# Kernel tuning notes

Hardware: AMD Instinct MI355X
Metric: run time of the kernel (lower is better)

The kernel has to match this reference:

```python
import jax, jax.numpy as jnp
import numpy as np

N_NODES = 50000
N_EDGES = 800000
D_IN, D_HID, D_OUT = 16, 64, 16
N_BLOCKS = 4


def setup_inputs() -> dict:
    key = jax.random.key(0)
    ks = jax.random.split(key, 12)
    s = 0.05  # small init scale to keep sum-aggregation over 4 blocks stable
    return {
        "x": jax.random.normal(ks[0], (N_NODES, D_IN), jnp.float32),
        "lframes": jax.random.normal(ks[1], (N_NODES, 4, 4), jnp.float32),
        "edge_index": jax.random.randint(ks[2], (2, N_EDGES), 0, N_NODES, jnp.int64),
        "lin_in_w": jax.random.normal(ks[3], (D_IN, D_HID), jnp.float32) * s,
        "lin_in_b": jnp.zeros((D_HID,), jnp.float32),
        # per-block mlp1: Linear(2D->D), ReLU, Linear(D->D), ReLU, Linear(D->D)
        "w0": jax.random.normal(ks[4], (N_BLOCKS, 2 * D_HID, D_HID), jnp.float32) * s,
        "b0": jnp.zeros((N_BLOCKS, D_HID), jnp.float32),
        "w1": jax.random.normal(ks[5], (N_BLOCKS, D_HID, D_HID), jnp.float32) * s,
        "b1": jnp.zeros((N_BLOCKS, D_HID), jnp.float32),
        "w2": jax.random.normal(ks[6], (N_BLOCKS, D_HID, D_HID), jnp.float32) * s,
        "b2": jnp.zeros((N_BLOCKS, D_HID), jnp.float32),
        "lin_out_w": jax.random.normal(ks[7], (D_HID, D_OUT), jnp.float32) * s,
        "lin_out_b": jnp.zeros((D_OUT,), jnp.float32),
    }


def reference(x, lframes, edge_index, lin_in_w, lin_in_b,
              w0, b0, w1, b1, w2, b2, lin_out_w, lin_out_b):
    src = edge_index[0]  # x_j (source / neighbor)
    dst = edge_index[1]  # x_i (target / aggregation node)
    h = x @ lin_in_w + lin_in_b  # [N, D]
    for k in range(N_BLOCKS):
        # message: cat((x_j, x_i)) -> mlp1 ; mlp2 is Identity (num_layers_mlp2=0)
        m = jnp.concatenate((h[src], h[dst]), axis=-1)  # [E, 2D]
        m = jax.nn.relu(m @ w0[k] + b0[k])
        m = jax.nn.relu(m @ w1[k] + b1[k])
        m = m @ w2[k] + b2[k]  # [E, D]
        # aggregate: scatter-add at target node
        h = jax.ops.segment_sum(m, dst, num_segments=N_NODES)
    return h @ lin_out_w + lin_out_b  # [N, D_OUT]
```

## Files before the change

### kernel.cpp

```cpp
#include <hip/hip_runtime.h>
#include <hip/hip_bf16.h>

#define N_NODES 50000
#define N_EDGES 800000
#define D_IN    16
#define D_HID   64
#define D_OUT   16
#define NCHUNK  ((N_NODES + 255) / 256)
#define TMAX    100352
#define GE4     ((N_EDGES / 4 + 255) / 256)
#define GH      ((N_NODES * D_HID + 255) / 256)

typedef __hip_bfloat16 bf16;
typedef _Float16 f16;
typedef _Float16 f16x8 __attribute__((ext_vector_type(8)));
typedef float    f32x4 __attribute__((ext_vector_type(4)));
typedef _Float16 f16x8a __attribute__((ext_vector_type(8), may_alias));

__device__ __forceinline__ float b2f(bf16 v) { return __bfloat162float(v); }
__device__ __forceinline__ int clampn(int v) {
    return v < 0 ? 0 : (v >= N_NODES ? N_NODES - 1 : v);
}
__device__ __forceinline__ float rdf(const void* p, long i, int isbf) {
    return isbf ? b2f(((const bf16*)p)[i]) : ((const float*)p)[i];
}
__device__ __forceinline__ f16x8 relu8(f16x8 v) {
#pragma unroll
    for (int j = 0; j < 8; j++) v[j] = v[j] > (f16)0 ? v[j] : (f16)0;
    return v;
}

__global__ __launch_bounds__(256) void k_detect(const unsigned short* __restrict__ xw,
                                                const int* __restrict__ ei,
                                                int* __restrict__ flags,
                                                int* __restrict__ hist)
{
    int i = blockIdx.x * 256 + threadIdx.x;
    if (i < N_NODES) hist[i] = 0;
    if (blockIdx.x == 0 && threadIdx.x == 0) {
        int inband = 0;
        for (int j = 0; j < 256; j++) {
            unsigned short w = xw[2 * j];
            int e = (w >> 7) & 0xFF;
            if ((w & 0x7FFF) == 0 || (e >= 100 && e <= 140)) inband++;
        }
        flags[0] = (inband >= 192) ? 1 : 0;
        int z = 1;
        for (int j = 1; j < 128; j += 2) z &= (ei[j] == 0) ? 1 : 0;
        flags[1] = z;
    }
}

__global__ __launch_bounds__(256) void k_prep(const int* __restrict__ flags,
                                              const void* __restrict__ gw0,
                                              const void* __restrict__ gw1,
                                              const void* __restrict__ gw2,
                                              f16* __restrict__ wfrag,
                                              const int* __restrict__ eidx,
                                              int* __restrict__ hist,
                                              const void* __restrict__ x,
                                              const void* __restrict__ liw,
                                              const void* __restrict__ lib,
                                              float* __restrict__ h)
{
    const int isbf = flags[0];
    const int bid = blockIdx.x;
    if (bid < 32) {
        int idx = bid * 256 + threadIdx.x;
        int kb = idx >> 11, rem = idx & 2047;
        int slot = rem >> 6, lane = rem & 63;
        int lm = lane & 15, quad = lane >> 4;
        f16* outp = wfrag + (long)idx * 8;
        if (slot < 16) {
            int c = slot >> 2, q = slot & 3;
            long base = (long)kb * 2 * D_HID * D_HID;
#pragma unroll
            for (int j = 0; j < 8; j++)
                outp[j] = (f16)rdf(gw0, base + (long)(c * 32 + quad * 8 + j) * 64 + q * 16 + lm, isbf);
        } else {
            const void* gw = (slot < 24) ? gw1 : gw2;
            int s = (slot < 24) ? slot - 16 : slot - 24;
            int c = s >> 2, q = s & 3;
            long base = (long)kb * D_HID * D_HID;
#pragma unroll
            for (int j = 0; j < 8; j++)
                outp[j] = (f16)rdf(gw, base + (long)(c * 32 + quad * 8 + j) * 64 + q * 16 + lm, isbf);
        }
    } else if (bid < 32 + GE4) {
        int base = ((bid - 32) * 256 + threadIdx.x) * 4;
        if (base >= N_EDGES) return;
        const int strd = flags[1] ? 2 : 1;
        const long dbase = flags[1] ? (long)(2 * N_EDGES) : (long)N_EDGES;
#pragma unroll
        for (int j = 0; j < 4; j++) {
            int e = base + j;
            if (e < N_EDGES)
                atomicAdd(&hist[clampn(eidx[dbase + (long)e * strd])], 1);
        }
    } else {
        int idx = (bid - 32 - GE4) * 256 + threadIdx.x;
        if (idx >= N_NODES * D_HID) return;
        int n = idx >> 6, c = idx & 63;
        float acc = rdf(lib, c, isbf);
#pragma unroll
        for (int i = 0; i < D_IN; i++)
            acc += rdf(x, (long)n * D_IN + i, isbf) * rdf(liw, (long)i * D_HID + c, isbf);
        h[idx] = acc;
    }
}

__global__ __launch_bounds__(256) void k_scan1(const int* __restrict__ hist,
                                               int* __restrict__ bsum_e,
                                               int* __restrict__ bsum_t)
{
    __shared__ int re[256], rt[256];
    const int t = threadIdx.x;
    int i = blockIdx.x * 256 + t;
    int v = (i < N_NODES) ? hist[i] : 0;
    re[t] = v; rt[t] = (v + 15) >> 4;
    __syncthreads();
    for (int d = 128; d > 0; d >>= 1) {
        if (t < d) { re[t] += re[t + d]; rt[t] += rt[t + d]; }
        __syncthreads();
    }
    if (t == 0) { bsum_e[blockIdx.x] = re[0]; bsum_t[blockIdx.x] = rt[0]; }
}

__global__ __launch_bounds__(256) void k_scan2(const int* __restrict__ bsum_e,
                                               const int* __restrict__ bsum_t,
                                               int* __restrict__ boff_e,
                                               int* __restrict__ boff_t,
                                               int* __restrict__ tot_e,
                                               int* __restrict__ tot_t)
{
    __shared__ int se[256], st_[256];
    const int t = threadIdx.x;
    se[t]  = (t < NCHUNK) ? bsum_e[t] : 0;
    st_[t] = (t < NCHUNK) ? bsum_t[t] : 0;
    __syncthreads();
    for (int d = 1; d < 256; d <<= 1) {
        int ve = (t >= d) ? se[t - d] : 0;
        int vt = (t >= d) ? st_[t - d] : 0;
        __syncthreads();
        se[t] += ve; st_[t] += vt;
        __syncthreads();
    }
    if (t < NCHUNK) {
        boff_e[t] = (t == 0) ? 0 : se[t - 1];
        boff_t[t] = (t == 0) ? 0 : st_[t - 1];
    }
    if (t == NCHUNK - 1) { tot_e[0] = se[t]; tot_t[0] = st_[t]; }
}

__global__ __launch_bounds__(256) void k_scan3(const int* __restrict__ hist,
                                               const int* __restrict__ boff_e,
                                               const int* __restrict__ boff_t,
                                               int* __restrict__ off,
                                               int* __restrict__ cursor,
                                               int* __restrict__ toff,
                                               int* __restrict__ tmeta)
{
    __shared__ int se[256], st_[256];
    const int t = threadIdx.x;
    int i = blockIdx.x * 256 + t;
    int v = (i < N_NODES) ? hist[i] : 0;
    int w = (v + 15) >> 4;
    se[t] = v; st_[t] = w;
    __syncthreads();
    for (int d = 1; d < 256; d <<= 1) {
        int ue = (t >= d) ? se[t - d] : 0;
        int ut = (t >= d) ? st_[t - d] : 0;
        __syncthreads();
        se[t] += ue; st_[t] += ut;
        __syncthreads();
    }
    if (i < N_NODES) {
        int exE = boff_e[blockIdx.x] + se[t] - v;
        off[i] = exE; cursor[i] = exE;
        int exT = boff_t[blockIdx.x] + st_[t] - w;
        toff[i] = exT;
        for (int j = 0; j < w; j++)
            tmeta[exT + j] = i | (min(16, v - 16 * j) << 20);
    }
}

__global__ __launch_bounds__(256) void k_scatter4(const int* __restrict__ flags,
                                                  const int* __restrict__ eidx,
                                                  int* __restrict__ cursor,
                                                  int* __restrict__ ssrc)
{
    int base = (blockIdx.x * 256 + threadIdx.x) * 4;
    if (base >= N_EDGES) return;
    const int strd = flags[1] ? 2 : 1;
    const long dbase = flags[1] ? (long)(2 * N_EDGES) : (long)N_EDGES;
    int d[4], s[4], pos[4], cnt = min(4, N_EDGES - base);
#pragma unroll
    for (int j = 0; j < 4; j++)
        if (j < cnt) {
            d[j] = clampn(eidx[dbase + (long)(base + j) * strd]);
            s[j] = clampn(eidx[(long)(base + j) * strd]);
        }
#pragma unroll
    for (int j = 0; j < 4; j++)
        if (j < cnt) pos[j] = atomicAdd(&cursor[d[j]], 1);
#pragma unroll
    for (int j = 0; j < 4; j++)
        if (j < cnt) ssrc[pos[j]] = s[j];
}

__global__ __launch_bounds__(256) void k_fill(const int* __restrict__ hist,
                                              const int* __restrict__ off,
                                              const int* __restrict__ toff,
                                              const int* __restrict__ totalp,
                                              const int* __restrict__ tmeta,
                                              const int* __restrict__ ssrc,
                                              int* __restrict__ spad)
{
    int idx = blockIdx.x * 256 + threadIdx.x;
    int t = idx >> 4, i = idx & 15;
    if (t >= totalp[0]) return;
    int n = tmeta[t] & 0xFFFFF;
    int j = t - toff[n];
    int dg = hist[n];
    spad[idx] = ssrc[off[n] + min(16 * j + i, dg - 1)];
}

#define HP_ST 72

__global__ __launch_bounds__(256) void k_proj(
    const int* __restrict__ flags, float* hio,
    const f16* __restrict__ wfrag, const void* __restrict__ gb0,
    const int* __restrict__ hist,
    f16* __restrict__ psrc, f16* __restrict__ pdst, int kblk)
{
    __shared__ f16 hL_s[4][16 * HP_ST];

    const int tid  = threadIdx.x;
    const int isbf = flags[0];
    const int wv = tid >> 6, ln = tid & 63;
    const int lm = ln & 15, quad = ln >> 4;
    f16* hL = hL_s[wv];

    const int g = blockIdx.x * 4 + wv;
    if (g >= N_NODES / 16) return;
    const int n0 = g * 16;

    const f16* wb = wfrag + (long)kblk * 32 * 64 * 8;

#pragma unroll
    for (int i = 0; i < 16; i++) {
        int idx = i * 64 + ln;
        hL[(idx >> 6) * HP_ST + (idx & 63)] = (f16)hio[(long)n0 * 64 + idx];
    }
#pragma unroll
    for (int i = 0; i < 16; i++)
        if (hist[n0 + i] == 0) hio[(long)(n0 + i) * 64 + ln] = 0.f;

    f16x8 a[2];
#pragma unroll
    for (int c = 0; c < 2; c++)
        a[c] = *(const f16x8a*)&hL[lm * HP_ST + c * 32 + quad * 8];

    f32x4 accS[4], accD[4];
#pragma unroll
    for (int q = 0; q < 4; q++) {
        float bd = rdf(gb0, (long)kblk * 64 + q * 16 + lm, isbf);
        accS[q] = (f32x4){0.f, 0.f, 0.f, 0.f};
        accD[q] = (f32x4){bd, bd, bd, bd};
    }
#pragma unroll
    for (int c = 0; c < 2; c++)
#pragma unroll
        for (int q = 0; q < 4; q++) {
            f16x8 bs = *(const f16x8a*)&wb[(((c + 0) * 4 + q) * 64 + ln) * 8];
            f16x8 bd = *(const f16x8a*)&wb[(((c + 2) * 4 + q) * 64 + ln) * 8];
            accS[q] = __builtin_amdgcn_mfma_f32_16x16x32_f16(a[c], bs, accS[q], 0, 0, 0);
            accD[q] = __builtin_amdgcn_mfma_f32_16x16x32_f16(a[c], bd, accD[q], 0, 0, 0);
        }
#pragma unroll
    for (int q = 0; q < 4; q++)
#pragma unroll
        for (int r = 0; r < 4; r++) {
            long o = (long)(n0 + quad * 4 + r) * 64 + q * 16 + lm;
            psrc[o] = (f16)accS[q][r];
            pdst[o] = (f16)accD[q][r];
        }
}

#define Y_ST 72

__global__ __launch_bounds__(256) void k_edge_tile(
    const int* __restrict__ flags,
    const int* __restrict__ ssrc_pad, const int* __restrict__ tmeta,
    const int* __restrict__ toff,
    const f16* __restrict__ psrc, const f16* __restrict__ pdst,
    float* __restrict__ hout,
    const f16* __restrict__ wfrag, const void* __restrict__ gb1,
    const void* __restrict__ gb2, int kblk)
{
    __shared__ f16 y_s[4][2][16 * Y_ST];

    const int tid  = threadIdx.x;
    const int isbf = flags[0];
    const int wv = tid >> 6, ln = tid & 63;
    const int lm = ln & 15, quad = ln >> 4;

    const f16* wb = wfrag + (long)kblk * 32 * 64 * 8;
    f16x8 bw1[2][4], bw2[2][4];
#pragma unroll
    for (int c = 0; c < 2; c++)
#pragma unroll
        for (int q = 0; q < 4; q++) {
            bw1[c][q] = *(const f16x8a*)&wb[((16 + c * 4 + q) * 64 + ln) * 8];
            bw2[c][q] = *(const f16x8a*)&wb[((24 + c * 4 + q) * 64 + ln) * 8];
        }
    float bias1[4], bias2[4];
#pragma unroll
    for (int q = 0; q < 4; q++) {
        bias1[q] = rdf(gb1, (long)kblk * 64 + q * 16 + lm, isbf);
        bias2[q] = rdf(gb2, (long)kblk * 64 + q * 16 + lm, isbf);
    }

    f16* yA = y_s[wv][0];
    f16* yB = y_s[wv][1];
    const int sub = ln & 7, eh = ln >> 3;

    const int T  = toff[N_NODES];
    const int W  = gridDim.x * 4;
    const int gw = blockIdx.x * 4 + wv;
    int t0 = (int)((long)gw * T / W);
    int t1 = (int)((long)(gw + 1) * T / W);
    if (t0 > 0)
        while (t0 < T && (tmeta[t0] & 0xFFFFF) == (tmeta[t0 - 1] & 0xFFFFF)) t0++;
    if (t1 > 0)
        while (t1 < T && (tmeta[t1] & 0xFFFFF) == (tmeta[t1 - 1] & 0xFFFFF)) t1++;
    if (t0 >= t1) return;

    int tcA = t0, tcB = min(t0 + 1, T - 1);
    int tc2 = min(t0 + 2, T - 1), tc3 = min(t0 + 3, T - 1);
    int m0 = tmeta[tcA], m1 = tmeta[tcB], m2 = tmeta[tc2], m3 = tmeta[tc3];
    int s2a = ssrc_pad[tc2 * 16 + eh], s2b = ssrc_pad[tc2 * 16 + 8 + eh];
    int s3a = ssrc_pad[tc3 * 16 + eh], s3b = ssrc_pad[tc3 * 16 + 8 + eh];
    int s0a = ssrc_pad[tcA * 16 + eh], s0b = ssrc_pad[tcA * 16 + 8 + eh];
    int s1a = ssrc_pad[tcB * 16 + eh], s1b = ssrc_pad[tcB * 16 + 8 + eh];
    f16x8 ps0a = *(const f16x8a*)&psrc[(long)s0a * 64 + sub * 8];
    f16x8 ps0b = *(const f16x8a*)&psrc[(long)s0b * 64 + sub * 8];
    f16x8 pd0  = *(const f16x8a*)&pdst[(long)(m0 & 0xFFFFF) * 64 + sub * 8];
    f16x8 ps1a = *(const f16x8a*)&psrc[(long)s1a * 64 + sub * 8];
    f16x8 ps1b = *(const f16x8a*)&psrc[(long)s1b * 64 + sub * 8];
    f16x8 pd1  = *(const f16x8a*)&pdst[(long)(m1 & 0xFFFFF) * 64 + sub * 8];

    float accn[4] = {0.f, 0.f, 0.f, 0.f};

    for (int tt = t0; tt < t1; tt += 2) {
        const int tc4 = min(tt + 4, T - 1), tc5 = min(tt + 5, T - 1);
        int m4 = tmeta[tc4], m5 = tmeta[tc5];
        int s4a = ssrc_pad[tc4 * 16 + eh], s4b = ssrc_pad[tc4 * 16 + 8 + eh];
        int s5a = ssrc_pad[tc5 * 16 + eh], s5b = ssrc_pad[tc5 * 16 + 8 + eh];
        f16x8 ps2a = *(const f16x8a*)&psrc[(long)s2a * 64 + sub * 8];
        f16x8 ps2b = *(const f16x8a*)&psrc[(long)s2b * 64 + sub * 8];
        f16x8 pd2  = *(const f16x8a*)&pdst[(long)(m2 & 0xFFFFF) * 64 + sub * 8];
        f16x8 ps3a = *(const f16x8a*)&psrc[(long)s3a * 64 + sub * 8];
        f16x8 ps3b = *(const f16x8a*)&psrc[(long)s3b * 64 + sub * 8];
        f16x8 pd3  = *(const f16x8a*)&pdst[(long)(m3 & 0xFFFFF) * 64 + sub * 8];

        const int hasB = (tt + 1 < t1);
        const int v0 = m0 >> 20;
        const int v1 = hasB ? (m1 >> 20) : 0;

        *(f16x8a*)&yA[eh * Y_ST + sub * 8]       = relu8(ps0a + pd0);
        *(f16x8a*)&yA[(8 + eh) * Y_ST + sub * 8] = relu8(ps0b + pd0);
        *(f16x8a*)&yB[eh * Y_ST + sub * 8]       = relu8(ps1a + pd1);
        *(f16x8a*)&yB[(8 + eh) * Y_ST + sub * 8] = relu8(ps1b + pd1);

        f16x8 a1A[2], a1B[2];
#pragma unroll
        for (int c = 0; c < 2; c++) {
            a1A[c] = *(const f16x8a*)&yA[lm * Y_ST + c * 32 + quad * 8];
            a1B[c] = *(const f16x8a*)&yB[lm * Y_ST + c * 32 + quad * 8];
        }
        f32x4 accA[4], accB[4];
#pragma unroll
        for (int q = 0; q < 4; q++) {
            accA[q] = (f32x4){bias1[q], bias1[q], bias1[q], bias1[q]};
            accB[q] = (f32x4){bias1[q], bias1[q], bias1[q], bias1[q]};
        }
#pragma unroll
        for (int c = 0; c < 2; c++)
#pragma unroll
            for (int q = 0; q < 4; q++) {
                accA[q] = __builtin_amdgcn_mfma_f32_16x16x32_f16(a1A[c], bw1[c][q], accA[q], 0, 0, 0);
                accB[q] = __builtin_amdgcn_mfma_f32_16x16x32_f16(a1B[c], bw1[c][q], accB[q], 0, 0, 0);
            }
#pragma unroll
        for (int q = 0; q < 4; q++)
#pragma unroll
            for (int r = 0; r < 4; r++) {
                yA[(quad * 4 + r) * Y_ST + q * 16 + lm] = (f16)fmaxf(accA[q][r], 0.f);
                yB[(quad * 4 + r) * Y_ST + q * 16 + lm] = (f16)fmaxf(accB[q][r], 0.f);
            }

        f16x8 a2A[2], a2B[2];
#pragma unroll
        for (int c = 0; c < 2; c++) {
            a2A[c] = *(const f16x8a*)&yA[lm * Y_ST + c * 32 + quad * 8];
            a2B[c] = *(const f16x8a*)&yB[lm * Y_ST + c * 32 + quad * 8];
        }
#pragma unroll
        for (int q = 0; q < 4; q++) {
            accA[q] = (f32x4){bias2[q], bias2[q], bias2[q], bias2[q]};
            accB[q] = (f32x4){bias2[q], bias2[q], bias2[q], bias2[q]};
        }
#pragma unroll
        for (int c = 0; c < 2; c++)
#pragma unroll
            for (int q = 0; q < 4; q++) {
                accA[q] = __builtin_amdgcn_mfma_f32_16x16x32_f16(a2A[c], bw2[c][q], accA[q], 0, 0, 0);
                accB[q] = __builtin_amdgcn_mfma_f32_16x16x32_f16(a2B[c], bw2[c][q], accB[q], 0, 0, 0);
            }

#pragma unroll
        for (int q = 0; q < 4; q++)
#pragma unroll
            for (int r = 0; r < 4; r++)
                if (quad * 4 + r < v0) accn[q] += accA[q][r];
        {
            const int curn = m0 & 0xFFFFF;
            const int nxt  = hasB ? (m1 & 0xFFFFF) : -1;
            if (nxt != curn) {
#pragma unroll
                for (int q = 0; q < 4; q++) {
                    float v = accn[q];
                    v += __shfl_xor(v, 16, 64);
                    v += __shfl_xor(v, 32, 64);
                    if (quad == 0) hout[(long)curn * 64 + q * 16 + lm] = v;
                    accn[q] = 0.f;
                }
            }
        }
        if (hasB) {
#pragma unroll
            for (int q = 0; q < 4; q++)
#pragma unroll
                for (int r = 0; r < 4; r++)
                    if (quad * 4 + r < v1) accn[q] += accB[q][r];
            const int curn = m1 & 0xFFFFF;
            const int nxt  = (tt + 2 < t1) ? (m2 & 0xFFFFF) : -1;
            if (nxt != curn) {
#pragma unroll
                for (int q = 0; q < 4; q++) {
                    float v = accn[q];
                    v += __shfl_xor(v, 16, 64);
                    v += __shfl_xor(v, 32, 64);
                    if (quad == 0) hout[(long)curn * 64 + q * 16 + lm] = v;
                    accn[q] = 0.f;
                }
            }
        }

        m0 = m2; m1 = m3; m2 = m4; m3 = m5;
        s2a = s4a; s2b = s4b; s3a = s5a; s3b = s5b;
        ps0a = ps2a; ps0b = ps2b; pd0 = pd2;
        ps1a = ps3a; ps1b = ps3b; pd1 = pd3;
    }
}

__global__ __launch_bounds__(256) void k_lin_out(const int* __restrict__ flags,
                                                 const float* __restrict__ h,
                                                 const void* __restrict__ w,
                                                 const void* __restrict__ b,
                                                 float* __restrict__ out)
{
    int idx = blockIdx.x * 256 + threadIdx.x;
    if (idx >= N_NODES * D_OUT) return;
    const int isbf = flags[0];
    int n = idx >> 4, c = idx & 15;
    float acc = rdf(b, c, isbf);
    const float* hr = h + (long)n * D_HID;
#pragma unroll
    for (int i = 0; i < D_HID; i++) acc += hr[i] * rdf(w, (long)i * D_OUT + c, isbf);
    out[idx] = acc;
}

extern "C" void kernel_launch(void* const* d_in, const int* in_sizes, int n_in,
                              void* d_out, int out_size, void* d_ws, size_t ws_size,
                              hipStream_t stream)
{
    const void* x    = d_in[0];
    const int*  ei   = (const int*)d_in[2];
    const void* liw  = d_in[3];
    const void* lib  = d_in[4];
    const void* w0   = d_in[5];
    const void* b0   = d_in[6];
    const void* w1   = d_in[7];
    const void* b1   = d_in[8];
    const void* w2   = d_in[9];
    const void* b2   = d_in[10];
    const void* low  = d_in[11];
    const void* lob  = d_in[12];
    float* out = (float*)d_out;

    char* wp = (char*)d_ws;
    int*   flags  = (int*)wp;                 wp += 256;
    float* hA     = (float*)wp;               wp += (size_t)N_NODES * D_HID * 4;
    f16*   Psrc   = (f16*)wp;                 wp += (size_t)N_NODES * D_HID * 2;
    f16*   Pdst   = (f16*)wp;                 wp += (size_t)N_NODES * D_HID * 2;
    f16*   wfrag  = (f16*)wp;                 wp += (size_t)4 * 32 * 64 * 8 * 2;
    int*   hist   = (int*)wp;                 wp += (size_t)N_NODES * 4;
    int*   off    = (int*)wp;                 wp += ((size_t)N_NODES + 1) * 4;
    int*   cursor = (int*)wp;                 wp += (size_t)N_NODES * 4;
    int*   toff   = (int*)wp;                 wp += ((size_t)N_NODES + 1) * 4;
    int*   bsum_e = (int*)wp;                 wp += 256 * 4;
    int*   bsum_t = (int*)wp;                 wp += 256 * 4;
    int*   boff_e = (int*)wp;                 wp += 256 * 4;
    int*   boff_t = (int*)wp;                 wp += 256 * 4;
    int*   ssrc   = (int*)wp;                 wp += (size_t)N_EDGES * 4;
    int*   tmeta  = (int*)wp;                 wp += (size_t)TMAX * 4;
    int*   spad   = (int*)wp;

    k_detect<<<NCHUNK, 256, 0, stream>>>((const unsigned short*)x, ei, flags, hist);
    k_prep<<<32 + GE4 + GH, 256, 0, stream>>>(flags, w0, w1, w2, wfrag,
                                              ei, hist, x, liw, lib, hA);

    k_scan1<<<NCHUNK, 256, 0, stream>>>(hist, bsum_e, bsum_t);
    k_scan2<<<1, 256, 0, stream>>>(bsum_e, bsum_t, boff_e, boff_t,
                                   off + N_NODES, toff + N_NODES);
    k_scan3<<<NCHUNK, 256, 0, stream>>>(hist, boff_e, boff_t, off, cursor, toff, tmeta);
    k_scatter4<<<(N_EDGES / 4 + 255) / 256, 256, 0, stream>>>(flags, ei, cursor, ssrc);
    k_fill<<<(TMAX * 16) / 256, 256, 0, stream>>>(hist, off, toff, toff + N_NODES,
                                                  tmeta, ssrc, spad);

    for (int k = 0; k < 4; k++) {
        k_proj<<<(N_NODES / 16 + 3) / 4, 256, 0, stream>>>(flags, hA, wfrag, b0,
                                                           hist, Psrc, Pdst, k);
        k_edge_tile<<<1024, 256, 0, stream>>>(flags, spad, tmeta, toff,
                                              Psrc, Pdst, hA, wfrag, b1, b2, k);
    }

    k_lin_out<<<(N_NODES * D_OUT + 255) / 256, 256, 0, stream>>>(flags, hA, low, lob, out);
}
```

Measured before the change: 455.0 us.

## Pad edge tiles with -inf sentinel node and subtract constant padding contribution

Padded edge slots now point to a sentinel row of Psrc filled with -inf f16. After ReLU, such a slot's layer-1 input is zero, so its final MLP output is a constant vector, which is precomputed per block. The per-row valid-edge masking in the accumulation is dropped, and the node sum is corrected by subtracting (16 - valid) times that constant. The edge loop also goes from two tiles per iteration with deep prefetch to one tile with one-ahead prefetch, using half the LDS, with launch bounds raised to 5 blocks per CU for occupancy. The trade-off is less latency hiding per wave and a result that depends on f16 rounding of the constant matching the MFMA path.

```diff
diff --git a/kernel.cpp b/kernel.cpp
--- a/kernel.cpp
+++ b/kernel.cpp
@@ -61,7 +61,10 @@
                                               const void* __restrict__ x,
                                               const void* __restrict__ liw,
                                               const void* __restrict__ lib,
-                                              float* __restrict__ h)
+                                              float* __restrict__ h,
+                                              const void* __restrict__ gb1,
+                                              const void* __restrict__ gb2,
+                                              float* __restrict__ cpad)
 {
     const int isbf = flags[0];
     const int bid = blockIdx.x;
@@ -97,7 +100,7 @@
             if (e < N_EDGES)
                 atomicAdd(&hist[clampn(eidx[dbase + (long)e * strd])], 1);
         }
-    } else {
+    } else if (bid < 32 + GE4 + GH) {
         int idx = (bid - 32 - GE4) * 256 + threadIdx.x;
         if (idx >= N_NODES * D_HID) return;
         int n = idx >> 6, c = idx & 63;
@@ -106,6 +109,16 @@
         for (int i = 0; i < D_IN; i++)
             acc += rdf(x, (long)n * D_IN + i, isbf) * rdf(liw, (long)i * D_HID + c, isbf);
         h[idx] = acc;
+    } else {
+        int t = threadIdx.x;
+        int k = t >> 6, j = t & 63;
+        float acc = rdf(gb2, (long)k * 64 + j, isbf);
+        for (int i = 0; i < 64; i++) {
+            float zi = (float)(f16)fmaxf(rdf(gb1, (long)k * 64 + i, isbf), 0.f);
+            float wi = (float)(f16)rdf(gw2, (long)k * 4096 + (long)i * 64 + j, isbf);
+            acc += zi * wi;
+        }
+        cpad[k * 64 + j] = acc;
     }
 }
 
@@ -214,15 +227,19 @@
                                               const int* __restrict__ totalp,
                                               const int* __restrict__ tmeta,
                                               const int* __restrict__ ssrc,
-                                              int* __restrict__ spad)
-{
+                                              int* __restrict__ spad,
+                                              unsigned short* __restrict__ psrc_us)
+{
+    if (blockIdx.x == 0 && threadIdx.x < 64)
+        psrc_us[(size_t)N_NODES * 64 + threadIdx.x] = 0xFC00u;
     int idx = blockIdx.x * 256 + threadIdx.x;
     int t = idx >> 4, i = idx & 15;
     if (t >= totalp[0]) return;
     int n = tmeta[t] & 0xFFFFF;
     int j = t - toff[n];
     int dg = hist[n];
-    spad[idx] = ssrc[off[n] + min(16 * j + i, dg - 1)];
+    int e = 16 * j + i;
+    spad[idx] = (e < dg) ? ssrc[off[n] + e] : N_NODES;
 }
 
 #define HP_ST 72
@@ -289,21 +306,23 @@
 
 #define Y_ST 72
 
-__global__ __launch_bounds__(256) void k_edge_tile(
+__global__ __launch_bounds__(256, 5) void k_edge_tile(
     const int* __restrict__ flags,
     const int* __restrict__ ssrc_pad, const int* __restrict__ tmeta,
     const int* __restrict__ toff,
     const f16* __restrict__ psrc, const f16* __restrict__ pdst,
     float* __restrict__ hout,
     const f16* __restrict__ wfrag, const void* __restrict__ gb1,
-    const void* __restrict__ gb2, int kblk)
-{
-    __shared__ f16 y_s[4][2][16 * Y_ST];
+    const void* __restrict__ gb2, const float* __restrict__ cpad, int kblk)
+{
+    __shared__ f16 y_s[4][16 * Y_ST];
 
     const int tid  = threadIdx.x;
     const int isbf = flags[0];
     const int wv = tid >> 6, ln = tid & 63;
     const int lm = ln & 15, quad = ln >> 4;
+    const int sub = ln & 7, eh = ln >> 3;
+    f16* y = y_s[wv];
 
     const f16* wb = wfrag + (long)kblk * 32 * 64 * 8;
     f16x8 bw1[2][4], bw2[2][4];
@@ -314,16 +333,13 @@
             bw1[c][q] = *(const f16x8a*)&wb[((16 + c * 4 + q) * 64 + ln) * 8];
             bw2[c][q] = *(const f16x8a*)&wb[((24 + c * 4 + q) * 64 + ln) * 8];
         }
-    float bias1[4], bias2[4];
+    float bias1[4], bias2[4], cp[4];
 #pragma unroll
     for (int q = 0; q < 4; q++) {
         bias1[q] = rdf(gb1, (long)kblk * 64 + q * 16 + lm, isbf);
         bias2[q] = rdf(gb2, (long)kblk * 64 + q * 16 + lm, isbf);
-    }
-
-    f16* yA = y_s[wv][0];
-    f16* yB = y_s[wv][1];
-    const int sub = ln & 7, eh = ln >> 3;
+        cp[q]    = cpad[kblk * 64 + q * 16 + lm];
+    }
 
     const int T  = toff[N_NODES];
     const int W  = gridDim.x * 4;
@@ -336,132 +352,80 @@
         while (t1 < T && (tmeta[t1] & 0xFFFFF) == (tmeta[t1 - 1] & 0xFFFFF)) t1++;
     if (t0 >= t1) return;
 
-    int tcA = t0, tcB = min(t0 + 1, T - 1);
-    int tc2 = min(t0 + 2, T - 1), tc3 = min(t0 + 3, T - 1);
-    int m0 = tmeta[tcA], m1 = tmeta[tcB], m2 = tmeta[tc2], m3 = tmeta[tc3];
-    int s2a = ssrc_pad[tc2 * 16 + eh], s2b = ssrc_pad[tc2 * 16 + 8 + eh];
-    int s3a = ssrc_pad[tc3 * 16 + eh], s3b = ssrc_pad[tc3 * 16 + 8 + eh];
-    int s0a = ssrc_pad[tcA * 16 + eh], s0b = ssrc_pad[tcA * 16 + 8 + eh];
+    const int tcB = min(t0 + 1, T - 1);
+    int m0 = tmeta[t0], m1 = tmeta[tcB];
     int s1a = ssrc_pad[tcB * 16 + eh], s1b = ssrc_pad[tcB * 16 + 8 + eh];
+    int s0a = ssrc_pad[t0 * 16 + eh],  s0b = ssrc_pad[t0 * 16 + 8 + eh];
     f16x8 ps0a = *(const f16x8a*)&psrc[(long)s0a * 64 + sub * 8];
     f16x8 ps0b = *(const f16x8a*)&psrc[(long)s0b * 64 + sub * 8];
     f16x8 pd0  = *(const f16x8a*)&pdst[(long)(m0 & 0xFFFFF) * 64 + sub * 8];
-    f16x8 ps1a = *(const f16x8a*)&psrc[(long)s1a * 64 + sub * 8];
-    f16x8 ps1b = *(const f16x8a*)&psrc[(long)s1b * 64 + sub * 8];
-    f16x8 pd1  = *(const f16x8a*)&pdst[(long)(m1 & 0xFFFFF) * 64 + sub * 8];
 
     float accn[4] = {0.f, 0.f, 0.f, 0.f};
 
-    for (int tt = t0; tt < t1; tt += 2) {
-        const int tc4 = min(tt + 4, T - 1), tc5 = min(tt + 5, T - 1);
-        int m4 = tmeta[tc4], m5 = tmeta[tc5];
-        int s4a = ssrc_pad[tc4 * 16 + eh], s4b = ssrc_pad[tc4 * 16 + 8 + eh];
-        int s5a = ssrc_pad[tc5 * 16 + eh], s5b = ssrc_pad[tc5 * 16 + 8 + eh];
-        f16x8 ps2a = *(const f16x8a*)&psrc[(long)s2a * 64 + sub * 8];
-        f16x8 ps2b = *(const f16x8a*)&psrc[(long)s2b * 64 + sub * 8];
-        f16x8 pd2  = *(const f16x8a*)&pdst[(long)(m2 & 0xFFFFF) * 64 + sub * 8];
-        f16x8 ps3a = *(const f16x8a*)&psrc[(long)s3a * 64 + sub * 8];
-        f16x8 ps3b = *(const f16x8a*)&psrc[(long)s3b * 64 + sub * 8];
-        f16x8 pd3  = *(const f16x8a*)&pdst[(long)(m3 & 0xFFFFF) * 64 + sub * 8];
-
-        const int hasB = (tt + 1 < t1);
-        const int v0 = m0 >> 20;
-        const int v1 = hasB ? (m1 >> 20) : 0;
-
-        *(f16x8a*)&yA[eh * Y_ST + sub * 8]       = relu8(ps0a + pd0);
-        *(f16x8a*)&yA[(8 + eh) * Y_ST + sub * 8] = relu8(ps0b + pd0);
-        *(f16x8a*)&yB[eh * Y_ST + sub * 8]       = relu8(ps1a + pd1);
-        *(f16x8a*)&yB[(8 + eh) * Y_ST + sub * 8] = relu8(ps1b + pd1);
-
-        f16x8 a1A[2], a1B[2];
-#pragma unroll
-        for (int c = 0; c < 2; c++) {
-            a1A[c] = *(const f16x8a*)&yA[lm * Y_ST + c * 32 + quad * 8];
-            a1B[c] = *(const f16x8a*)&yB[lm * Y_ST + c * 32 + quad * 8];
-        }
-        f32x4 accA[4], accB[4];
-#pragma unroll
-        for (int q = 0; q < 4; q++) {
-            accA[q] = (f32x4){bias1[q], bias1[q], bias1[q], bias1[q]};
-            accB[q] = (f32x4){bias1[q], bias1[q], bias1[q], bias1[q]};
-        }
+    for (int tt = t0; tt < t1; ++tt) {
+        const int tc2 = min(tt + 2, T - 1);
+        const int m2  = tmeta[tc2];
+        const int s2a = ssrc_pad[tc2 * 16 + eh], s2b = ssrc_pad[tc2 * 16 + 8 + eh];
+        f16x8 ps1a = *(const f16x8a*)&psrc[(long)s1a * 64 + sub * 8];
+        f16x8 ps1b = *(const f16x8a*)&psrc[(long)s1b * 64 + sub * 8];
+        f16x8 pd1  = *(const f16x8a*)&pdst[(long)(m1 & 0xFFFFF) * 64 + sub * 8];
+
+        *(f16x8a*)&y[eh * Y_ST + sub * 8]       = relu8(ps0a + pd0);
+        *(f16x8a*)&y[(8 + eh) * Y_ST + sub * 8] = relu8(ps0b + pd0);
+
+        f16x8 a1[2];
+        a1[0] = *(const f16x8a*)&y[lm * Y_ST + quad * 8];
+        a1[1] = *(const f16x8a*)&y[lm * Y_ST + 32 + quad * 8];
+        f32x4 acc[4];
+#pragma unroll
+        for (int q = 0; q < 4; q++)
+            acc[q] = (f32x4){bias1[q], bias1[q], bias1[q], bias1[q]};
 #pragma unroll
         for (int c = 0; c < 2; c++)
 #pragma unroll
+            for (int q = 0; q < 4; q++)
+                acc[q] = __builtin_amdgcn_mfma_f32_16x16x32_f16(a1[c], bw1[c][q], acc[q], 0, 0, 0);
+#pragma unroll
+        for (int q = 0; q < 4; q++)
+#pragma unroll
+            for (int r = 0; r < 4; r++)
+                y[(quad * 4 + r) * Y_ST + q * 16 + lm] = (f16)fmaxf(acc[q][r], 0.f);
+
+        f16x8 a2[2];
+        a2[0] = *(const f16x8a*)&y[lm * Y_ST + quad * 8];
+        a2[1] = *(const f16x8a*)&y[lm * Y_ST + 32 + quad * 8];
+#pragma unroll
+        for (int q = 0; q < 4; q++)
+            acc[q] = (f32x4){bias2[q], bias2[q], bias2[q], bias2[q]};
+#pragma unroll
+        for (int c = 0; c < 2; c++)
+#pragma unroll
+            for (int q = 0; q < 4; q++)
+                acc[q] = __builtin_amdgcn_mfma_f32_16x16x32_f16(a2[c], bw2[c][q], acc[q], 0, 0, 0);
+
+#pragma unroll
+        for (int q = 0; q < 4; q++)
+#pragma unroll
+            for (int r = 0; r < 4; r++)
+                accn[q] += acc[q][r];
+
+        const int curn = m0 & 0xFFFFF;
+        const int nxt  = (tt + 1 < t1) ? (m1 & 0xFFFFF) : -1;
+        if (nxt != curn) {
+            const float npad = (float)(16 - (m0 >> 20));
+#pragma unroll
             for (int q = 0; q < 4; q++) {
-                accA[q] = __builtin_amdgcn_mfma_f32_16x16x32_f16(a1A[c], bw1[c][q], accA[q], 0, 0, 0);
-                accB[q] = __builtin_amdgcn_mfma_f32_16x16x32_f16(a1B[c], bw1[c][q], accB[q], 0, 0, 0);
+                float v = accn[q];
+                v += __shfl_xor(v, 16, 64);
+                v += __shfl_xor(v, 32, 64);
+                if (quad == 0) hout[(long)curn * 64 + q * 16 + lm] = v - npad * cp[q];
+                accn[q] = 0.f;
             }
-#pragma unroll
-        for (int q = 0; q < 4; q++)
-#pragma unroll
-            for (int r = 0; r < 4; r++) {
-                yA[(quad * 4 + r) * Y_ST + q * 16 + lm] = (f16)fmaxf(accA[q][r], 0.f);
-                yB[(quad * 4 + r) * Y_ST + q * 16 + lm] = (f16)fmaxf(accB[q][r], 0.f);
-            }
-
-        f16x8 a2A[2], a2B[2];
-#pragma unroll
-        for (int c = 0; c < 2; c++) {
-            a2A[c] = *(const f16x8a*)&yA[lm * Y_ST + c * 32 + quad * 8];
-            a2B[c] = *(const f16x8a*)&yB[lm * Y_ST + c * 32 + quad * 8];
-        }
-#pragma unroll
-        for (int q = 0; q < 4; q++) {
-            accA[q] = (f32x4){bias2[q], bias2[q], bias2[q], bias2[q]};
-            accB[q] = (f32x4){bias2[q], bias2[q], bias2[q], bias2[q]};
-        }
-#pragma unroll
-        for (int c = 0; c < 2; c++)
-#pragma unroll
-            for (int q = 0; q < 4; q++) {
-                accA[q] = __builtin_amdgcn_mfma_f32_16x16x32_f16(a2A[c], bw2[c][q], accA[q], 0, 0, 0);
-                accB[q] = __builtin_amdgcn_mfma_f32_16x16x32_f16(a2B[c], bw2[c][q], accB[q], 0, 0, 0);
-            }
-
-#pragma unroll
-        for (int q = 0; q < 4; q++)
-#pragma unroll
-            for (int r = 0; r < 4; r++)
-                if (quad * 4 + r < v0) accn[q] += accA[q][r];
-        {
-            const int curn = m0 & 0xFFFFF;
-            const int nxt  = hasB ? (m1 & 0xFFFFF) : -1;
-            if (nxt != curn) {
-#pragma unroll
-                for (int q = 0; q < 4; q++) {
-                    float v = accn[q];
-                    v += __shfl_xor(v, 16, 64);
-                    v += __shfl_xor(v, 32, 64);
-                    if (quad == 0) hout[(long)curn * 64 + q * 16 + lm] = v;
-                    accn[q] = 0.f;
-                }
-            }
-        }
-        if (hasB) {
-#pragma unroll
-            for (int q = 0; q < 4; q++)
-#pragma unroll
-                for (int r = 0; r < 4; r++)
-                    if (quad * 4 + r < v1) accn[q] += accB[q][r];
-            const int curn = m1 & 0xFFFFF;
-            const int nxt  = (tt + 2 < t1) ? (m2 & 0xFFFFF) : -1;
-            if (nxt != curn) {
-#pragma unroll
-                for (int q = 0; q < 4; q++) {
-                    float v = accn[q];
-                    v += __shfl_xor(v, 16, 64);
-                    v += __shfl_xor(v, 32, 64);
-                    if (quad == 0) hout[(long)curn * 64 + q * 16 + lm] = v;
-                    accn[q] = 0.f;
-                }
-            }
-        }
-
-        m0 = m2; m1 = m3; m2 = m4; m3 = m5;
-        s2a = s4a; s2b = s4b; s3a = s5a; s3b = s5b;
-        ps0a = ps2a; ps0b = ps2b; pd0 = pd2;
-        ps1a = ps3a; ps1b = ps3b; pd1 = pd3;
+        }
+
+        m0 = m1; m1 = m2;
+        s1a = s2a; s1b = s2b;
+        ps0a = ps1a; ps0b = ps1b; pd0 = pd1;
     }
 }
 
@@ -503,9 +467,10 @@
     char* wp = (char*)d_ws;
     int*   flags  = (int*)wp;                 wp += 256;
     float* hA     = (float*)wp;               wp += (size_t)N_NODES * D_HID * 4;
-    f16*   Psrc   = (f16*)wp;                 wp += (size_t)N_NODES * D_HID * 2;
+    f16*   Psrc   = (f16*)wp;                 wp += ((size_t)N_NODES + 1) * D_HID * 2;
     f16*   Pdst   = (f16*)wp;                 wp += (size_t)N_NODES * D_HID * 2;
     f16*   wfrag  = (f16*)wp;                 wp += (size_t)4 * 32 * 64 * 8 * 2;
+    float* cpad   = (float*)wp;               wp += (size_t)4 * 64 * 4;
     int*   hist   = (int*)wp;                 wp += (size_t)N_NODES * 4;
     int*   off    = (int*)wp;                 wp += ((size_t)N_NODES + 1) * 4;
     int*   cursor = (int*)wp;                 wp += (size_t)N_NODES * 4;
@@ -519,8 +484,9 @@
     int*   spad   = (int*)wp;
 
     k_detect<<<NCHUNK, 256, 0, stream>>>((const unsigned short*)x, ei, flags, hist);
-    k_prep<<<32 + GE4 + GH, 256, 0, stream>>>(flags, w0, w1, w2, wfrag,
-                                              ei, hist, x, liw, lib, hA);
+    k_prep<<<32 + GE4 + GH + 1, 256, 0, stream>>>(flags, w0, w1, w2, wfrag,
+                                                  ei, hist, x, liw, lib, hA,
+                                                  b1, b2, cpad);
 
     k_scan1<<<NCHUNK, 256, 0, stream>>>(hist, bsum_e, bsum_t);
     k_scan2<<<1, 256, 0, stream>>>(bsum_e, bsum_t, boff_e, boff_t,
@@ -528,13 +494,15 @@
     k_scan3<<<NCHUNK, 256, 0, stream>>>(hist, boff_e, boff_t, off, cursor, toff, tmeta);
     k_scatter4<<<(N_EDGES / 4 + 255) / 256, 256, 0, stream>>>(flags, ei, cursor, ssrc);
     k_fill<<<(TMAX * 16) / 256, 256, 0, stream>>>(hist, off, toff, toff + N_NODES,
-                                                  tmeta, ssrc, spad);
+                                                  tmeta, ssrc, spad,
+                                                  (unsigned short*)Psrc);
 
     for (int k = 0; k < 4; k++) {
         k_proj<<<(N_NODES / 16 + 3) / 4, 256, 0, stream>>>(flags, hA, wfrag, b0,
                                                            hist, Psrc, Pdst, k);
         k_edge_tile<<<1024, 256, 0, stream>>>(flags, spad, tmeta, toff,
-                                              Psrc, Pdst, hA, wfrag, b1, b2, k);
+                                              Psrc, Pdst, hA, wfrag, b1, b2,
+                                              cpad, k);
     }
 
     k_lin_out<<<(N_NODES * D_OUT + 255) / 256, 256, 0, stream>>>(flags, hA, low, lob, out);
```

After: 830.2 us. 82.5% more time.
